# Kernel optimization log

Hardware: AMD Instinct MI355X
Metric: run time of the kernel (lower is better)

The kernel has to match this reference:

```python
import jax, jax.numpy as jnp
import numpy as np

# Pool2d config (init_kwargs): 3x3 max pool, stride 2, symmetric pad 1, dilation 1
K = 3
STRIDE = 2
PAD = 1  # (left, right, top, bottom) all equal
DIL = 1
FILL = 0.0  # padding_fill_value


def setup_inputs() -> dict:
    key = jax.random.key(0)
    X = jax.random.normal(key, (32, 192, 224, 224), dtype=jnp.float32)  # NCHW
    return {"X": X}


def reference(X):
    # F.pad with constant padding_fill_value, then sliding-window max over KxK
    # (dilated) patches with the given stride -- same math as unfold + max
    # reduce over the patch axis, but without materializing K*K patches.
    Xp = jnp.pad(X, ((0, 0), (0, 0), (PAD, PAD), (PAD, PAD)), constant_values=FILL)
    Y = jax.lax.reduce_window(
        Xp,
        -jnp.inf,
        jax.lax.max,
        window_dimensions=(1, 1, K, K),
        window_strides=(1, 1, STRIDE, STRIDE),
        padding='VALID',
        window_dilation=(1, 1, DIL, DIL),
    )  # [N, C, H_out, W_out] = [32, 192, 112, 112]
    return Y
```

## Files before the change

### kernel.cpp

```cpp
#include <hip/hip_runtime.h>
#include <math.h>


namespace {
constexpr int H = 224;
constexpr int W = 224;
constexpr int HO = 112;
constexpr int WO = 112;
constexpr int QPR = WO / 4;
constexpr int NROWS = 32 * 192 * HO;
constexpr int TOTAL_QUADS = NROWS * QPR;
}

__global__ __launch_bounds__(256) void pool3x3s2_kernel(
    const float* __restrict__ X, float* __restrict__ Y) {
  const int stride = gridDim.x * blockDim.x;
  for (int idx = blockIdx.x * blockDim.x + threadIdx.x; idx < TOTAL_QUADS;
       idx += stride) {
    const int q   = idx % QPR;
    const int row = idx / QPR;
    const int oy  = row % HO;
    const int nc  = row / HO;

    const float* __restrict__ img = X + (size_t)nc * (H * W);
    const int iy0 = 2 * oy - 1;
    const int ixs = 8 * q;

    float m0 = -INFINITY, m1 = -INFINITY, m2 = -INFINITY, m3 = -INFINITY;

#pragma unroll
    for (int dy = 0; dy < 3; ++dy) {
      const int iy = iy0 + dy;
      float a, b0, b1, b2, b3, b4, b5, b6, b7;
      if (0 <= iy && iy < H) {
        const float* __restrict__ r = img + iy * W;
        a = (ixs > 0) ? r[ixs - 1] : 0.0f;
        const float4 v0 = *reinterpret_cast<const float4*>(r + ixs);
        const float4 v1 = *reinterpret_cast<const float4*>(r + ixs + 4);
        b0 = v0.x; b1 = v0.y; b2 = v0.z; b3 = v0.w;
        b4 = v1.x; b5 = v1.y; b6 = v1.z; b7 = v1.w;
      } else {
        a = b0 = b1 = b2 = b3 = b4 = b5 = b6 = b7 = 0.0f;
      }
      m0 = fmaxf(m0, fmaxf(a,  fmaxf(b0, b1)));
      m1 = fmaxf(m1, fmaxf(b1, fmaxf(b2, b3)));
      m2 = fmaxf(m2, fmaxf(b3, fmaxf(b4, b5)));
      m3 = fmaxf(m3, fmaxf(b5, fmaxf(b6, b7)));
    }

    float4 o;
    o.x = m0; o.y = m1; o.z = m2; o.w = m3;
    *reinterpret_cast<float4*>(Y + (size_t)row * WO + 4 * q) = o;
  }
}

extern "C" void kernel_launch(void* const* d_in, const int* in_sizes, int n_in,
                              void* d_out, int out_size, void* d_ws, size_t ws_size,
                              hipStream_t stream) {
  const float* X = (const float*)d_in[0];
  float* Y = (float*)d_out;
  pool3x3s2_kernel<<<2048, 256, 0, stream>>>(X, Y);
}
```

Measured before the change: 309.4 us.

## Compute two output rows and eight columns per thread to reuse shared input row

```diff
diff --git a/kernel.cpp b/kernel.cpp
--- a/kernel.cpp
+++ b/kernel.cpp
@@ -7,50 +7,66 @@
 constexpr int W = 224;
 constexpr int HO = 112;
 constexpr int WO = 112;
-constexpr int QPR = WO / 4;
-constexpr int NROWS = 32 * 192 * HO;
-constexpr int TOTAL_QUADS = NROWS * QPR;
+constexpr int GPR = WO / 8;
+constexpr int PAIRS = HO / 2;
+constexpr int NC = 32 * 192;
+constexpr int TOTAL = NC * PAIRS * GPR;
 }
 
 __global__ __launch_bounds__(256) void pool3x3s2_kernel(
     const float* __restrict__ X, float* __restrict__ Y) {
   const int stride = gridDim.x * blockDim.x;
-  for (int idx = blockIdx.x * blockDim.x + threadIdx.x; idx < TOTAL_QUADS;
+  for (int idx = blockIdx.x * blockDim.x + threadIdx.x; idx < TOTAL;
        idx += stride) {
-    const int q   = idx % QPR;
-    const int row = idx / QPR;
-    const int oy  = row % HO;
-    const int nc  = row / HO;
+    const int g  = idx % GPR;
+    const int t  = idx / GPR;
+    const int p  = t % PAIRS;
+    const int nc = t / PAIRS;
 
     const float* __restrict__ img = X + (size_t)nc * (H * W);
-    const int iy0 = 2 * oy - 1;
-    const int ixs = 8 * q;
+    const int ixs = 16 * g;
+    const int iy0 = 4 * p - 1;
 
-    float m0 = -INFINITY, m1 = -INFINITY, m2 = -INFINITY, m3 = -INFINITY;
+    float h[5][8];
 
 #pragma unroll
-    for (int dy = 0; dy < 3; ++dy) {
-      const int iy = iy0 + dy;
-      float a, b0, b1, b2, b3, b4, b5, b6, b7;
-      if (0 <= iy && iy < H) {
-        const float* __restrict__ r = img + iy * W;
-        a = (ixs > 0) ? r[ixs - 1] : 0.0f;
-        const float4 v0 = *reinterpret_cast<const float4*>(r + ixs);
-        const float4 v1 = *reinterpret_cast<const float4*>(r + ixs + 4);
-        b0 = v0.x; b1 = v0.y; b2 = v0.z; b3 = v0.w;
-        b4 = v1.x; b5 = v1.y; b6 = v1.z; b7 = v1.w;
+    for (int r = 0; r < 5; ++r) {
+      const int iy = iy0 + r;
+      float a, x[16];
+      if (iy >= 0) {
+        const float* __restrict__ row = img + iy * W + ixs;
+        const float4 v0 = *reinterpret_cast<const float4*>(row);
+        const float4 v1 = *reinterpret_cast<const float4*>(row + 4);
+        const float4 v2 = *reinterpret_cast<const float4*>(row + 8);
+        const float4 v3 = *reinterpret_cast<const float4*>(row + 12);
+        a = (ixs > 0) ? row[-1] : 0.0f;
+        x[0] = v0.x; x[1] = v0.y; x[2]  = v0.z; x[3]  = v0.w;
+        x[4] = v1.x; x[5] = v1.y; x[6]  = v1.z; x[7]  = v1.w;
+        x[8] = v2.x; x[9] = v2.y; x[10] = v2.z; x[11] = v2.w;
+        x[12] = v3.x; x[13] = v3.y; x[14] = v3.z; x[15] = v3.w;
       } else {
-        a = b0 = b1 = b2 = b3 = b4 = b5 = b6 = b7 = 0.0f;
+        a = 0.0f;
+#pragma unroll
+        for (int i = 0; i < 16; ++i) x[i] = 0.0f;
       }
-      m0 = fmaxf(m0, fmaxf(a,  fmaxf(b0, b1)));
-      m1 = fmaxf(m1, fmaxf(b1, fmaxf(b2, b3)));
-      m2 = fmaxf(m2, fmaxf(b3, fmaxf(b4, b5)));
-      m3 = fmaxf(m3, fmaxf(b5, fmaxf(b6, b7)));
+      h[r][0] = fmaxf(fmaxf(a, x[0]), x[1]);
+#pragma unroll
+      for (int j = 1; j < 8; ++j)
+        h[r][j] = fmaxf(fmaxf(x[2 * j - 1], x[2 * j]), x[2 * j + 1]);
     }
 
-    float4 o;
-    o.x = m0; o.y = m1; o.z = m2; o.w = m3;
-    *reinterpret_cast<float4*>(Y + (size_t)row * WO + 4 * q) = o;
+    float o0[8], o1[8];
+#pragma unroll
+    for (int j = 0; j < 8; ++j) {
+      o0[j] = fmaxf(fmaxf(h[0][j], h[1][j]), h[2][j]);
+      o1[j] = fmaxf(fmaxf(h[2][j], h[3][j]), h[4][j]);
+    }
+
+    float* __restrict__ out = Y + ((size_t)nc * HO + 2 * p) * WO + 8 * g;
+    *reinterpret_cast<float4*>(out)          = make_float4(o0[0], o0[1], o0[2], o0[3]);
+    *reinterpret_cast<float4*>(out + 4)      = make_float4(o0[4], o0[5], o0[6], o0[7]);
+    *reinterpret_cast<float4*>(out + WO)     = make_float4(o1[0], o1[1], o1[2], o1[3]);
+    *reinterpret_cast<float4*>(out + WO + 4) = make_float4(o1[4], o1[5], o1[6], o1[7]);
   }
 }
 
```

After: 321.1 us. 3.8% more time.

## Stream one channel per wavefront, reusing rows vertically in registers

Applied to the files above, without the earlier changes.

```diff
diff --git a/kernel.cpp b/kernel.cpp
--- a/kernel.cpp
+++ b/kernel.cpp
@@ -7,50 +7,49 @@
 constexpr int W = 224;
 constexpr int HO = 112;
 constexpr int WO = 112;
-constexpr int QPR = WO / 4;
-constexpr int NROWS = 32 * 192 * HO;
-constexpr int TOTAL_QUADS = NROWS * QPR;
+constexpr int NC = 32 * 192;
 }
 
-__global__ __launch_bounds__(256) void pool3x3s2_kernel(
+__global__ __launch_bounds__(256) void pool3x3s2_stream(
     const float* __restrict__ X, float* __restrict__ Y) {
-  const int stride = gridDim.x * blockDim.x;
-  for (int idx = blockIdx.x * blockDim.x + threadIdx.x; idx < TOTAL_QUADS;
-       idx += stride) {
-    const int q   = idx % QPR;
-    const int row = idx / QPR;
-    const int oy  = row % HO;
-    const int nc  = row / HO;
+  const int gtid = blockIdx.x * blockDim.x + threadIdx.x;
+  const int ch   = gtid >> 6;
+  const int lane = threadIdx.x & 63;
+  if (ch >= NC) return;
 
-    const float* __restrict__ img = X + (size_t)nc * (H * W);
-    const int iy0 = 2 * oy - 1;
-    const int ixs = 8 * q;
+  const float* __restrict__ img = X + (size_t)ch * (H * W);
+  float* __restrict__ out = Y + (size_t)ch * (HO * WO);
 
-    float m0 = -INFINITY, m1 = -INFINITY, m2 = -INFINITY, m3 = -INFINITY;
+  const bool active = lane < 56;
+  const float* __restrict__ p = img + 4 * lane;
 
-#pragma unroll
-    for (int dy = 0; dy < 3; ++dy) {
-      const int iy = iy0 + dy;
-      float a, b0, b1, b2, b3, b4, b5, b6, b7;
-      if (0 <= iy && iy < H) {
-        const float* __restrict__ r = img + iy * W;
-        a = (ixs > 0) ? r[ixs - 1] : 0.0f;
-        const float4 v0 = *reinterpret_cast<const float4*>(r + ixs);
-        const float4 v1 = *reinterpret_cast<const float4*>(r + ixs + 4);
-        b0 = v0.x; b1 = v0.y; b2 = v0.z; b3 = v0.w;
-        b4 = v1.x; b5 = v1.y; b6 = v1.z; b7 = v1.w;
-      } else {
-        a = b0 = b1 = b2 = b3 = b4 = b5 = b6 = b7 = 0.0f;
-      }
-      m0 = fmaxf(m0, fmaxf(a,  fmaxf(b0, b1)));
-      m1 = fmaxf(m1, fmaxf(b1, fmaxf(b2, b3)));
-      m2 = fmaxf(m2, fmaxf(b3, fmaxf(b4, b5)));
-      m3 = fmaxf(m3, fmaxf(b5, fmaxf(b6, b7)));
-    }
+  float2 hprev = make_float2(0.0f, 0.0f);
 
-    float4 o;
-    o.x = m0; o.y = m1; o.z = m2; o.w = m3;
-    *reinterpret_cast<float4*>(Y + (size_t)row * WO + 4 * q) = o;
+#pragma unroll 4
+  for (int r = 0; r < H; r += 2) {
+    float4 v = active ? *reinterpret_cast<const float4*>(p)
+                      : make_float4(0.f, 0.f, 0.f, 0.f);
+    float4 w = active ? *reinterpret_cast<const float4*>(p + W)
+                      : make_float4(0.f, 0.f, 0.f, 0.f);
+    p += 2 * W;
+
+    float vm1 = __shfl_up(v.w, 1);
+    float wm1 = __shfl_up(w.w, 1);
+    if (lane == 0) { vm1 = 0.0f; wm1 = 0.0f; }
+
+    float2 hv, hw;
+    hv.x = fmaxf(fmaxf(vm1, v.x), v.y);
+    hv.y = fmaxf(fmaxf(v.y, v.z), v.w);
+    hw.x = fmaxf(fmaxf(wm1, w.x), w.y);
+    hw.y = fmaxf(fmaxf(w.y, w.z), w.w);
+
+    float2 o;
+    o.x = fmaxf(fmaxf(hprev.x, hv.x), hw.x);
+    o.y = fmaxf(fmaxf(hprev.y, hv.y), hw.y);
+    if (active)
+      *reinterpret_cast<float2*>(out + (r >> 1) * WO + 2 * lane) = o;
+
+    hprev = hw;
   }
 }
 
@@ -59,5 +58,5 @@
                               hipStream_t stream) {
   const float* X = (const float*)d_in[0];
   float* Y = (float*)d_out;
-  pool3x3s2_kernel<<<2048, 256, 0, stream>>>(X, Y);
+  pool3x3s2_stream<<<NC / 4, 256, 0, stream>>>(X, Y);
 }
```

Result: slower. 324.6 us (+4.9%).

## Compute 2x4 output tile per thread with shared row reuse and nontemporal stores

Applied to the files above, without the earlier changes.

```diff
diff --git a/kernel.cpp b/kernel.cpp
--- a/kernel.cpp
+++ b/kernel.cpp
@@ -8,50 +8,59 @@
 constexpr int HO = 112;
 constexpr int WO = 112;
 constexpr int QPR = WO / 4;
-constexpr int NROWS = 32 * 192 * HO;
-constexpr int TOTAL_QUADS = NROWS * QPR;
+constexpr int PAIRS = HO / 2;
+constexpr int NC = 32 * 192;
+constexpr int TOTAL = NC * PAIRS * QPR;
+
+typedef float v4f __attribute__((ext_vector_type(4)));
 }
 
-__global__ __launch_bounds__(256) void pool3x3s2_kernel(
+__global__ __launch_bounds__(256) void pool3x3s2_tile2x4(
     const float* __restrict__ X, float* __restrict__ Y) {
-  const int stride = gridDim.x * blockDim.x;
-  for (int idx = blockIdx.x * blockDim.x + threadIdx.x; idx < TOTAL_QUADS;
-       idx += stride) {
-    const int q   = idx % QPR;
-    const int row = idx / QPR;
-    const int oy  = row % HO;
-    const int nc  = row / HO;
+  const int idx = blockIdx.x * blockDim.x + threadIdx.x;
+  const int q  = idx % QPR;
+  const int t  = idx / QPR;
+  const int p  = t % PAIRS;
+  const int nc = t / PAIRS;
 
-    const float* __restrict__ img = X + (size_t)nc * (H * W);
-    const int iy0 = 2 * oy - 1;
-    const int ixs = 8 * q;
+  const float* __restrict__ img = X + (size_t)nc * (H * W);
+  const int ixs = 8 * q;
+  const int iy0 = 4 * p - 1;
 
-    float m0 = -INFINITY, m1 = -INFINITY, m2 = -INFINITY, m3 = -INFINITY;
+  float h[5][4];
+#pragma unroll
+  for (int r = 0; r < 5; ++r) {
+    const int iy = iy0 + r;
+    float a, b0, b1, b2, b3, b4, b5, b6, b7;
+    if (iy >= 0) {
+      const float* __restrict__ row = img + iy * W + ixs;
+      a = (ixs > 0) ? row[-1] : 0.0f;
+      const v4f v0 = *reinterpret_cast<const v4f*>(row);
+      const v4f v1 = *reinterpret_cast<const v4f*>(row + 4);
+      b0 = v0.x; b1 = v0.y; b2 = v0.z; b3 = v0.w;
+      b4 = v1.x; b5 = v1.y; b6 = v1.z; b7 = v1.w;
+    } else {
+      a = b0 = b1 = b2 = b3 = b4 = b5 = b6 = b7 = 0.0f;
+    }
+    h[r][0] = fmaxf(fmaxf(a,  b0), b1);
+    h[r][1] = fmaxf(fmaxf(b1, b2), b3);
+    h[r][2] = fmaxf(fmaxf(b3, b4), b5);
+    h[r][3] = fmaxf(fmaxf(b5, b6), b7);
+  }
 
-#pragma unroll
-    for (int dy = 0; dy < 3; ++dy) {
-      const int iy = iy0 + dy;
-      float a, b0, b1, b2, b3, b4, b5, b6, b7;
-      if (0 <= iy && iy < H) {
-        const float* __restrict__ r = img + iy * W;
-        a = (ixs > 0) ? r[ixs - 1] : 0.0f;
-        const float4 v0 = *reinterpret_cast<const float4*>(r + ixs);
-        const float4 v1 = *reinterpret_cast<const float4*>(r + ixs + 4);
-        b0 = v0.x; b1 = v0.y; b2 = v0.z; b3 = v0.w;
-        b4 = v1.x; b5 = v1.y; b6 = v1.z; b7 = v1.w;
-      } else {
-        a = b0 = b1 = b2 = b3 = b4 = b5 = b6 = b7 = 0.0f;
-      }
-      m0 = fmaxf(m0, fmaxf(a,  fmaxf(b0, b1)));
-      m1 = fmaxf(m1, fmaxf(b1, fmaxf(b2, b3)));
-      m2 = fmaxf(m2, fmaxf(b3, fmaxf(b4, b5)));
-      m3 = fmaxf(m3, fmaxf(b5, fmaxf(b6, b7)));
-    }
+  v4f o0, o1;
+  o0.x = fmaxf(fmaxf(h[0][0], h[1][0]), h[2][0]);
+  o0.y = fmaxf(fmaxf(h[0][1], h[1][1]), h[2][1]);
+  o0.z = fmaxf(fmaxf(h[0][2], h[1][2]), h[2][2]);
+  o0.w = fmaxf(fmaxf(h[0][3], h[1][3]), h[2][3]);
+  o1.x = fmaxf(fmaxf(h[2][0], h[3][0]), h[4][0]);
+  o1.y = fmaxf(fmaxf(h[2][1], h[3][1]), h[4][1]);
+  o1.z = fmaxf(fmaxf(h[2][2], h[3][2]), h[4][2]);
+  o1.w = fmaxf(fmaxf(h[2][3], h[3][3]), h[4][3]);
 
-    float4 o;
-    o.x = m0; o.y = m1; o.z = m2; o.w = m3;
-    *reinterpret_cast<float4*>(Y + (size_t)row * WO + 4 * q) = o;
-  }
+  float* __restrict__ out = Y + ((size_t)nc * HO + 2 * p) * WO + 4 * q;
+  __builtin_nontemporal_store(o0, reinterpret_cast<v4f*>(out));
+  __builtin_nontemporal_store(o1, reinterpret_cast<v4f*>(out + WO));
 }
 
 extern "C" void kernel_launch(void* const* d_in, const int* in_sizes, int n_in,
@@ -59,5 +68,5 @@
                               hipStream_t stream) {
   const float* X = (const float*)d_in[0];
   float* Y = (float*)d_out;
-  pool3x3s2_kernel<<<2048, 256, 0, stream>>>(X, Y);
+  pool3x3s2_tile2x4<<<TOTAL / 256, 256, 0, stream>>>(X, Y);
 }
```

New measurement: 274.4 us. 1.13x faster.
